# Optimization experiments

Hardware: AMD Instinct MI355X
Metric: run time of the kernel (lower is better)

The kernel has to match this reference:

```python
import jax, jax.numpy as jnp
import numpy as np
import math

B, Q, K, D = 16, 2048, 2048, 128


def setup_inputs() -> dict:
    key = jax.random.key(0)
    k1, k2, k3, k4 = jax.random.split(key, 4)
    return {
        "queries": jax.random.normal(k1, (B, Q, D), dtype=jnp.float32),
        "keys": jax.random.normal(k2, (B, K, D), dtype=jnp.float32),
        "values": jax.random.normal(k3, (B, K, D), dtype=jnp.float32),
        "valid_lens": jax.random.randint(k4, (B,), 1, K + 1, dtype=jnp.int32),
    }


def reference(queries, keys, values, valid_lens):
    d = queries.shape[2]
    # scores: [B, Q, K]
    scores = jnp.einsum("bqd,bkd->bqk", queries, keys) / math.sqrt(d)
    # mask: arange(K) < valid_lens[b], broadcast over query dim -> [B, 1, K]
    mask = jnp.arange(scores.shape[-1])[None, None, :] < valid_lens[:, None, None]
    scores = jnp.where(mask, scores, jnp.float32(-1000000.0))
    weights = jax.nn.softmax(scores, axis=-1)
    return jnp.einsum("bqk,bkd->bqd", weights, values)
```

## Files before the change

kernel.cpp:

```cpp
#include <hip/hip_runtime.h>

typedef unsigned short u16;
typedef __bf16 bf16x8 __attribute__((ext_vector_type(8)));
typedef float f32x4 __attribute__((ext_vector_type(4)));

union B8 { uint4 u; bf16x8 v; };
union U8 { u16 s[8]; uint4 u; };

#define NQ 2048
#define NK 2048
#define ND 128

template<int C>
__device__ __forceinline__ float dppf(float x) {
  int v = __builtin_bit_cast(int, x);
  int r = __builtin_amdgcn_update_dpp(v, v, C, 0xF, 0xF, true);
  return __builtin_bit_cast(float, r);
}
__device__ __forceinline__ float rowmax16(float x) {
  x = fmaxf(x, dppf<0xB1>(x));
  x = fmaxf(x, dppf<0x4E>(x));
  x = fmaxf(x, dppf<0x141>(x));
  x = fmaxf(x, dppf<0x140>(x));
  return x;
}
__device__ __forceinline__ float rowsum16(float x) {
  x += dppf<0xB1>(x);
  x += dppf<0x4E>(x);
  x += dppf<0x141>(x);
  x += dppf<0x140>(x);
  return x;
}

__device__ __forceinline__ bf16x8 cvt8(float4 a, float4 b) {
  bf16x8 r;
  r[0] = (__bf16)a.x; r[1] = (__bf16)a.y; r[2] = (__bf16)a.z; r[3] = (__bf16)a.w;
  r[4] = (__bf16)b.x; r[5] = (__bf16)b.y; r[6] = (__bf16)b.z; r[7] = (__bf16)b.w;
  return r;
}

__device__ __forceinline__ void async16(const u16* g, u16* l) {
  __builtin_amdgcn_global_load_lds(
      (const __attribute__((address_space(1))) unsigned int*)g,
      (__attribute__((address_space(3))) unsigned int*)l, 16, 0, 0);
}

__global__ __launch_bounds__(256)
void prepack(const float* __restrict__ kg, const float* __restrict__ vg,
             u16* __restrict__ wk, u16* __restrict__ wvp)
{
  __shared__ __align__(16) u16 sVp[8192];
  const int bt  = blockIdx.x;
  const int tid = threadIdx.x;
  const int srow = tid >> 2, scq = tid & 3;
  const size_t rowoff = (size_t)((bt >> 5) * NK + (bt & 31) * 64 + srow) * ND + scq * 32;

  u16* kimg = wk + (size_t)bt * 8192;
  {
    const float* src = kg + rowoff;
    #pragma unroll
    for (int c = 0; c < 4; ++c) {
      B8 tt; tt.v = cvt8(*(const float4*)(src + c * 8), *(const float4*)(src + c * 8 + 4));
      *(uint4*)(&kimg[srow * 128 + (((scq * 4 + c) ^ (srow & 15)) << 3)]) = tt.u;
    }
  }
  {
    const float* src = vg + rowoff;
    #pragma unroll
    for (int c = 0; c < 4; ++c) {
      B8 x; x.v = cvt8(*(const float4*)(src + c * 8), *(const float4*)(src + c * 8 + 4));
      U8 tt; tt.u = x.u;
      #pragma unroll
      for (int j = 0; j < 8; ++j) {
        int d = scq * 32 + c * 8 + j;
        sVp[d * 64 + (((srow >> 3) ^ j) << 3) + (srow & 7)] = tt.s[j];
      }
    }
  }
  __syncthreads();
  u16* vimg = wvp + (size_t)bt * 8192;
  const uint4* s4 = (const uint4*)sVp;
  uint4* d4 = (uint4*)vimg;
  #pragma unroll
  for (int k = 0; k < 4; ++k) d4[tid + 256 * k] = s4[tid + 256 * k];
}

__global__ __launch_bounds__(512, 2)
void flash_fwd(const float* __restrict__ qg, const int* __restrict__ vlg,
               float* __restrict__ og,
               const u16* __restrict__ wk, const u16* __restrict__ wvp)
{
  __shared__ __align__(16) u16 smem[81920];
  u16* const sKb = smem;
  u16* const sVb = smem + 32768;
  u16* const sPb = smem + 65536;
  float* const fb = (float*)smem;

  const int tid  = threadIdx.x;
  const int lane = tid & 63;
  const int wv   = tid >> 6;
  const int qw   = wv & 3;
  const int grp  = wv >> 2;
  const int n    = lane & 15;
  const int quad = lane >> 4;

  const int bi = blockIdx.x;
  const int b  = ((bi & 7) << 1) | ((bi >> 3) & 1);
  const int qt = bi >> 4;

  const int vl = vlg[b];
  const int nt = (vl + 63) >> 6;

  const int qrow0 = qt * 128 + qw * 32;

  bf16x8 qf[2][4];
  #pragma unroll
  for (int mb = 0; mb < 2; ++mb)
    #pragma unroll
    for (int c = 0; c < 4; ++c) {
      const float* qp = qg + (size_t)(b * NQ + qrow0 + mb * 16 + n) * ND + c * 32 + quad * 8;
      qf[mb][c] = cvt8(*(const float4*)qp, *(const float4*)(qp + 4));
    }

  f32x4 O[2][8];
  float mst[2][4], lst[2][4];
  #pragma unroll
  for (int mb = 0; mb < 2; ++mb) {
    #pragma unroll
    for (int f = 0; f < 8; ++f) O[mb][f] = (f32x4){0.f, 0.f, 0.f, 0.f};
    #pragma unroll
    for (int r = 0; r < 4; ++r) { mst[mb][r] = -__builtin_inff(); lst[mb][r] = 0.f; }
  }

  #define STAGE(t, buf)                                                        \
    do {                                                                       \
      const size_t io_ = (size_t)(b * 32 + (t)) * 8192 + qw * 2048;            \
      const u16* gk_ = wk  + io_ + lane * 8;                                   \
      const u16* gv_ = wvp + io_ + lane * 8;                                   \
      u16* lk_ = sKb + (grp * 2 + (buf)) * 8192 + qw * 2048;                   \
      u16* lv_ = sVb + (grp * 2 + (buf)) * 8192 + qw * 2048;                   \
      _Pragma("unroll")                                                        \
      for (int j_ = 0; j_ < 4; ++j_) {                                         \
        async16(gk_ + j_ * 512, lk_ + j_ * 512 + lane * 8);                    \
        async16(gv_ + j_ * 512, lv_ + j_ * 512 + lane * 8);                    \
      }                                                                        \
    } while (0)

  u16* const Pw = sPb + wv * 2048;

  constexpr float CEXP = 0.08838834764831845f * 1.44269504088896340f;

  if (grp < nt) STAGE(grp, 0);

  const int NS = (nt + 1) >> 1;
  for (int i = 0; i < NS; ++i) {
    __syncthreads();
    const int t  = 2 * i + grp;
    const int tn = t + 2;
    if (tn < nt) STAGE(tn, (i + 1) & 1);

    if (t < nt) {
      const u16* Kg = sKb + (grp * 2 + (i & 1)) * 8192;
      const u16* Vg = sVb + (grp * 2 + (i & 1)) * 8192;

      f32x4 S[2][4];
      #pragma unroll
      for (int mb = 0; mb < 2; ++mb)
        #pragma unroll
        for (int jn = 0; jn < 4; ++jn) S[mb][jn] = (f32x4){0.f, 0.f, 0.f, 0.f};
      #pragma unroll
      for (int c = 0; c < 4; ++c)
        #pragma unroll
        for (int jn = 0; jn < 4; ++jn) {
          B8 bb;
          bb.u = *(const uint4*)(&Kg[(jn * 16 + n) * 128 + (((c * 4 + quad) ^ n) << 3)]);
          S[0][jn] = __builtin_amdgcn_mfma_f32_16x16x32_bf16(qf[0][c], bb.v, S[0][jn], 0, 0, 0);
          S[1][jn] = __builtin_amdgcn_mfma_f32_16x16x32_bf16(qf[1][c], bb.v, S[1][jn], 0, 0, 0);
        }

      if (t * 64 + 64 > vl) {
        #pragma unroll
        for (int jn = 0; jn < 4; ++jn) {
          const bool msk = (t * 64 + jn * 16 + n) >= vl;
          #pragma unroll
          for (int r = 0; r < 4; ++r) {
            S[0][jn][r] = msk ? -1e30f : S[0][jn][r];
            S[1][jn][r] = msk ? -1e30f : S[1][jn][r];
          }
        }
      }

      float al[2][4];
      #pragma unroll
      for (int mb = 0; mb < 2; ++mb)
        #pragma unroll
        for (int r = 0; r < 4; ++r) {
          float mx = fmaxf(fmaxf(S[mb][0][r], S[mb][1][r]), fmaxf(S[mb][2][r], S[mb][3][r]));
          mx = rowmax16(mx);
          float mnew = fmaxf(mst[mb][r], mx);
          float a = __builtin_exp2f((mst[mb][r] - mnew) * CEXP);
          mst[mb][r] = mnew;
          float ssum = 0.f;
          #pragma unroll
          for (int jn = 0; jn < 4; ++jn) {
            float p = __builtin_exp2f((S[mb][jn][r] - mnew) * CEXP);
            S[mb][jn][r] = p;
            ssum += p;
          }
          ssum = rowsum16(ssum);
          lst[mb][r] = lst[mb][r] * a + ssum;
          al[mb][r] = a;
        }
      #pragma unroll
      for (int mb = 0; mb < 2; ++mb)
        #pragma unroll
        for (int f = 0; f < 8; ++f) {
          O[mb][f][0] *= al[mb][0]; O[mb][f][1] *= al[mb][1];
          O[mb][f][2] *= al[mb][2]; O[mb][f][3] *= al[mb][3];
        }

      #pragma unroll
      for (int mb = 0; mb < 2; ++mb)
        #pragma unroll
        for (int jn = 0; jn < 4; ++jn)
          #pragma unroll
          for (int r = 0; r < 4; ++r) {
            int row = mb * 16 + quad * 4 + r;
            __bf16 h = (__bf16)S[mb][jn][r];
            Pw[row * 64 + (((jn * 2 + (n >> 3)) ^ (row & 7)) << 3) + (n & 7)]
                = __builtin_bit_cast(u16, h);
          }

      #pragma unroll
      for (int kc = 0; kc < 2; ++kc) {
        bf16x8 af[2];
        #pragma unroll
        for (int mb = 0; mb < 2; ++mb) {
          B8 ta;
          ta.u = *(const uint4*)(&Pw[(mb * 16 + n) * 64 + (((kc * 4 + quad) ^ (n & 7)) << 3)]);
          af[mb] = ta.v;
        }
        #pragma unroll
        for (int f = 0; f < 8; ++f) {
          int d = f * 16 + n;
          B8 bb;
          bb.u = *(const uint4*)(&Vg[d * 64 + (((kc * 4 + quad) ^ (n & 7)) << 3)]);
          O[0][f] = __builtin_amdgcn_mfma_f32_16x16x32_bf16(af[0], bb.v, O[0][f], 0, 0, 0);
          O[1][f] = __builtin_amdgcn_mfma_f32_16x16x32_bf16(af[1], bb.v, O[1][f], 0, 0, 0);
        }
      }
    }
  }
  #undef STAGE

  __syncthreads();
  float* const ps = fb + 16384;
  if (grp == 1) {
    #pragma unroll
    for (int mb = 0; mb < 2; ++mb) {
      #pragma unroll
      for (int f = 0; f < 8; ++f)
        #pragma unroll
        for (int r = 0; r < 4; ++r)
          fb[(qw * 32 + mb * 16 + quad * 4 + r) * 128 + f * 16 + n] = O[mb][f][r];
      if (n == 0) {
        #pragma unroll
        for (int r = 0; r < 4; ++r) {
          const int row = qw * 32 + mb * 16 + quad * 4 + r;
          ps[row * 2]     = mst[mb][r];
          ps[row * 2 + 1] = lst[mb][r];
        }
      }
    }
  }
  __syncthreads();
  if (grp == 0) {
    #pragma unroll
    for (int mb = 0; mb < 2; ++mb)
      #pragma unroll
      for (int r = 0; r < 4; ++r) {
        const int row = qw * 32 + mb * 16 + quad * 4 + r;
        const float m1 = ps[row * 2], l1 = ps[row * 2 + 1];
        const float m  = fmaxf(mst[mb][r], m1);
        const float a0 = __builtin_exp2f((mst[mb][r] - m) * CEXP);
        const float a1 = __builtin_exp2f((m1 - m) * CEXP);
        const float rl = 1.0f / (lst[mb][r] * a0 + l1 * a1);
        #pragma unroll
        for (int f = 0; f < 8; ++f) {
          const int idx = row * 128 + f * 16 + n;
          fb[idx] = (O[mb][f][r] * a0 + fb[idx] * a1) * rl;
        }
      }
  }
  __syncthreads();
  {
    const float4* s4 = (const float4*)fb;
    float4* d4 = (float4*)(og + (size_t)(b * NQ + qt * 128) * ND);
    #pragma unroll
    for (int k = 0; k < 8; ++k)
      d4[tid + 512 * k] = s4[tid + 512 * k];
  }
}

__global__ __launch_bounds__(1024)
void flash_fwd_fb(const float* __restrict__ qg, const float* __restrict__ kg,
                  const float* __restrict__ vg, const int* __restrict__ vlg,
                  float* __restrict__ og)
{
  __shared__ __align__(16) u16 sK[2][64 * 128];
  __shared__ __align__(16) u16 sV[2][64 * 128];
  __shared__ __align__(16) u16 sP[16][16 * 64];

  const int tid  = threadIdx.x;
  const int lane = tid & 63;
  const int wv   = tid >> 6;
  const int qw   = wv & 7;
  const int grp  = wv >> 3;
  const int n    = lane & 15;
  const int quad = lane >> 4;

  const int bi = blockIdx.x;
  const int b  = ((bi & 7) << 1) | ((bi >> 3) & 1);
  const int qt = bi >> 4;

  const int vl = vlg[b];
  const int nt = (vl + 63) >> 6;
  const int qrow0 = qt * 128 + qw * 16;

  bf16x8 qf[4];
  #pragma unroll
  for (int c = 0; c < 4; ++c) {
    const float* qp = qg + (size_t)(b * NQ + qrow0 + n) * ND + c * 32 + quad * 8;
    qf[c] = cvt8(*(const float4*)qp, *(const float4*)(qp + 4));
  }

  f32x4 O[8];
  float mst[4], lst[4];
  #pragma unroll
  for (int f = 0; f < 8; ++f) O[f] = (f32x4){0.f, 0.f, 0.f, 0.f};
  #pragma unroll
  for (int r = 0; r < 4; ++r) { mst[r] = -__builtin_inff(); lst[r] = 0.f; }

  const float* kb = kg + (size_t)(b * NK) * ND;
  const float* vb = vg + (size_t)(b * NK) * ND;
  const int stid = tid & 511;
  const int srow = stid >> 3, sc8 = stid & 7;
  bf16x8 kreg[2], vreg[2];

  auto kload = [&](int t) {
    const float* src = kb + (size_t)(t * 64 + srow) * ND + sc8 * 16;
    #pragma unroll
    for (int c = 0; c < 2; ++c)
      kreg[c] = cvt8(*(const float4*)(src + c * 8), *(const float4*)(src + c * 8 + 4));
  };
  auto kstore = [&]() {
    #pragma unroll
    for (int c = 0; c < 2; ++c) {
      B8 tt; tt.v = kreg[c];
      *(uint4*)(&sK[grp][srow * 128 + (((sc8 * 2 + c) ^ (srow & 15)) << 3)]) = tt.u;
    }
  };
  auto vload = [&](int t) {
    const float* src = vb + (size_t)(t * 64 + srow) * ND + sc8 * 16;
    #pragma unroll
    for (int c = 0; c < 2; ++c)
      vreg[c] = cvt8(*(const float4*)(src + c * 8), *(const float4*)(src + c * 8 + 4));
  };
  auto vstore = [&]() {
    #pragma unroll
    for (int c = 0; c < 2; ++c) {
      B8 x; x.v = vreg[c];
      U8 tt; tt.u = x.u;
      #pragma unroll
      for (int j = 0; j < 8; ++j) {
        int d = sc8 * 16 + c * 8 + j;
        sV[grp][d * 64 + (((srow >> 3) ^ j) << 3) + (srow & 7)] = tt.s[j];
      }
    }
  };

  if (grp < nt) { kload(grp); vload(grp); kstore(); vstore(); }

  constexpr float CEXP = 0.08838834764831845f * 1.44269504088896340f;
  u16* Pw = sP[wv];
  const u16* Kg = sK[grp];
  const u16* Vg = sV[grp];

  const int NS = (nt + 1) >> 1;
  for (int i = 0; i < NS; ++i) {
    __syncthreads();
    const int t  = 2 * i + grp;
    const int tn = t + 2;
    if (tn < nt) { kload(tn); vload(tn); }

    if (t < nt) {
      f32x4 S[4];
      #pragma unroll
      for (int jn = 0; jn < 4; ++jn) S[jn] = (f32x4){0.f, 0.f, 0.f, 0.f};
      #pragma unroll
      for (int c = 0; c < 4; ++c)
        #pragma unroll
        for (int jn = 0; jn < 4; ++jn) {
          B8 bb;
          bb.u = *(const uint4*)(&Kg[(jn * 16 + n) * 128 + (((c * 4 + quad) ^ n) << 3)]);
          S[jn] = __builtin_amdgcn_mfma_f32_16x16x32_bf16(qf[c], bb.v, S[jn], 0, 0, 0);
        }
      if (t * 64 + 64 > vl) {
        #pragma unroll
        for (int jn = 0; jn < 4; ++jn) {
          const bool msk = (t * 64 + jn * 16 + n) >= vl;
          #pragma unroll
          for (int r = 0; r < 4; ++r)
            S[jn][r] = msk ? -1e30f : S[jn][r];
        }
      }
      float al[4];
      #pragma unroll
      for (int r = 0; r < 4; ++r) {
        float mx = fmaxf(fmaxf(S[0][r], S[1][r]), fmaxf(S[2][r], S[3][r]));
        mx = rowmax16(mx);
        float mnew = fmaxf(mst[r], mx);
        float a = __builtin_exp2f((mst[r] - mnew) * CEXP);
        mst[r] = mnew;
        float ssum = 0.f;
        #pragma unroll
        for (int jn = 0; jn < 4; ++jn) {
          float p = __builtin_exp2f((S[jn][r] - mnew) * CEXP);
          S[jn][r] = p;
          ssum += p;
        }
        ssum = rowsum16(ssum);
        lst[r] = lst[r] * a + ssum;
        al[r] = a;
      }
      #pragma unroll
      for (int f = 0; f < 8; ++f) {
        O[f][0] *= al[0]; O[f][1] *= al[1]; O[f][2] *= al[2]; O[f][3] *= al[3];
      }
      #pragma unroll
      for (int jn = 0; jn < 4; ++jn)
        #pragma unroll
        for (int r = 0; r < 4; ++r) {
          int row = quad * 4 + r;
          __bf16 h = (__bf16)S[jn][r];
          Pw[row * 64 + (((jn * 2 + (n >> 3)) ^ (row & 7)) << 3) + (n & 7)]
              = __builtin_bit_cast(u16, h);
        }
      #pragma unroll
      for (int kc = 0; kc < 2; ++kc) {
        B8 ta;
        ta.u = *(const uint4*)(&Pw[n * 64 + (((kc * 4 + quad) ^ (n & 7)) << 3)]);
        bf16x8 af = ta.v;
        #pragma unroll
        for (int f = 0; f < 8; ++f) {
          int d = f * 16 + n;
          B8 bb;
          bb.u = *(const uint4*)(&Vg[d * 64 + (((kc * 4 + quad) ^ (n & 7)) << 3)]);
          O[f] = __builtin_amdgcn_mfma_f32_16x16x32_bf16(af, bb.v, O[f], 0, 0, 0);
        }
      }
    }
    __syncthreads();
    if (tn < nt) { kstore(); vstore(); }
  }

  if (grp == 1) {
    float* ob = ((qw < 4) ? (float*)sK : (float*)sV) + (qw & 3) * 2048 + lane * 32;
    #pragma unroll
    for (int f = 0; f < 8; ++f)
      #pragma unroll
      for (int r = 0; r < 4; ++r)
        ob[f * 4 + r] = O[f][r];
    float* sb = (float*)sP + qw * 512 + lane * 8;
    #pragma unroll
    for (int r = 0; r < 4; ++r) { sb[r] = mst[r]; sb[4 + r] = lst[r]; }
  }
  __syncthreads();
  if (grp == 0) {
    const float* ob = ((qw < 4) ? (const float*)sK : (const float*)sV) + (qw & 3) * 2048 + lane * 32;
    const float* sb = (const float*)sP + qw * 512 + lane * 8;
    #pragma unroll
    for (int r = 0; r < 4; ++r) {
      const float m1 = sb[r], l1 = sb[4 + r];
      const float m  = fmaxf(mst[r], m1);
      const float a0 = __builtin_exp2f((mst[r] - m) * CEXP);
      const float a1 = __builtin_exp2f((m1 - m) * CEXP);
      const float rl = 1.0f / (lst[r] * a0 + l1 * a1);
      const int qrow = qrow0 + quad * 4 + r;
      float* op = og + (size_t)(b * NQ + qrow) * ND + n;
      #pragma unroll
      for (int f = 0; f < 8; ++f)
        op[f * 16] = (O[f][r] * a0 + ob[f * 4 + r] * a1) * rl;
    }
  }
}

extern "C" void kernel_launch(void* const* d_in, const int* in_sizes, int n_in,
                              void* d_out, int out_size, void* d_ws, size_t ws_size,
                              hipStream_t stream) {
  const float* q  = (const float*)d_in[0];
  const float* k  = (const float*)d_in[1];
  const float* v  = (const float*)d_in[2];
  const int*  vl  = (const int*)d_in[3];
  float* out = (float*)d_out;

  const size_t need = (size_t)16 * 1024 * 1024;
  if (ws_size >= need) {
    u16* wk  = (u16*)d_ws;
    u16* wvv = wk + 4194304;
    hipLaunchKernelGGL(prepack, dim3(512), dim3(256), 0, stream, k, v, wk, wvv);
    hipLaunchKernelGGL(flash_fwd, dim3(256), dim3(512), 0, stream, q, vl, out, wk, wvv);
  } else {
    hipLaunchKernelGGL(flash_fwd_fb, dim3(256), dim3(1024), 0, stream, q, k, v, vl, out);
  }
}
```

Before: 162.6 us.

## Split attention over key chunks with a separate merge kernel

Adds a split-KV path: flash_chunk processes up to 8 key tiles per block across 1024 blocks, writing partial O plus per-row max and sum to workspace. A merge_chunks kernel then rescales and combines the partials. The aim is to balance work across CUs when valid_lens vary per batch and to raise occupancy, since the old grid of 256 blocks left the whole loop over keys to one block. The cost is an extra kernel launch, fp32 partial traffic through global memory, and a path that only runs when the workspace is large enough.

```diff
diff --git a/kernel.cpp b/kernel.cpp
--- a/kernel.cpp
+++ b/kernel.cpp
@@ -44,6 +44,8 @@
       (const __attribute__((address_space(1))) unsigned int*)g,
       (__attribute__((address_space(3))) unsigned int*)l, 16, 0, 0);
 }
+
+constexpr float CEXP = 0.08838834764831845f * 1.44269504088896340f;
 
 __global__ __launch_bounds__(256)
 void prepack(const float* __restrict__ kg, const float* __restrict__ vg,
@@ -83,6 +85,216 @@
   uint4* d4 = (uint4*)vimg;
   #pragma unroll
   for (int k = 0; k < 4; ++k) d4[tid + 256 * k] = s4[tid + 256 * k];
+}
+
+__global__ __launch_bounds__(512, 4)
+void flash_chunk(const float* __restrict__ qg, const int* __restrict__ vlg,
+                 const u16* __restrict__ wk, const u16* __restrict__ wvp,
+                 float* __restrict__ pO, float* __restrict__ pML)
+{
+  __shared__ __align__(16) u16 sK[2][8192];
+  __shared__ __align__(16) u16 sV[2][8192];
+  __shared__ __align__(16) u16 sP[8][1024];
+
+  const int tid  = threadIdx.x;
+  const int lane = tid & 63;
+  const int wv   = tid >> 6;
+  const int n    = lane & 15;
+  const int quad = lane >> 4;
+
+  const int bi   = blockIdx.x;
+  const int b    = ((bi & 7) << 1) | ((bi >> 3) & 1);
+  const int rest = bi >> 4;
+  const int qt   = rest & 15;
+  const int ck   = rest >> 4;
+
+  const int vl = vlg[b];
+  const int nt = (vl + 63) >> 6;
+  const int t0 = ck * 8;
+  if (t0 >= nt) return;
+  const int t1 = (t0 + 8 < nt) ? (t0 + 8) : nt;
+
+  const int qrow0 = qt * 128 + wv * 16;
+
+  bf16x8 qf[4];
+  #pragma unroll
+  for (int c = 0; c < 4; ++c) {
+    const float* qp = qg + (size_t)(b * NQ + qrow0 + n) * ND + c * 32 + quad * 8;
+    qf[c] = cvt8(*(const float4*)qp, *(const float4*)(qp + 4));
+  }
+
+  f32x4 O[8];
+  float mst[4], lst[4];
+  #pragma unroll
+  for (int f = 0; f < 8; ++f) O[f] = (f32x4){0.f, 0.f, 0.f, 0.f};
+  #pragma unroll
+  for (int r = 0; r < 4; ++r) { mst[r] = -__builtin_inff(); lst[r] = 0.f; }
+
+  #define STAGE(t, buf)                                                        \
+    do {                                                                       \
+      const size_t io_ = (size_t)(b * 32 + (t)) * 8192 + wv * 1024;            \
+      const u16* gk_ = wk  + io_ + lane * 8;                                   \
+      const u16* gv_ = wvp + io_ + lane * 8;                                   \
+      u16* lk_ = sK[(buf)] + wv * 1024 + lane * 8;                             \
+      u16* lv_ = sV[(buf)] + wv * 1024 + lane * 8;                             \
+      async16(gk_,       lk_);                                                 \
+      async16(gk_ + 512, lk_ + 512);                                           \
+      async16(gv_,       lv_);                                                 \
+      async16(gv_ + 512, lv_ + 512);                                           \
+    } while (0)
+
+  u16* const Pw = sP[wv];
+
+  STAGE(t0, 0);
+
+  for (int t = t0; t < t1; ++t) {
+    __syncthreads();
+    if (t + 1 < t1) STAGE(t + 1, (t - t0 + 1) & 1);
+
+    const u16* Kg = sK[(t - t0) & 1];
+    const u16* Vg = sV[(t - t0) & 1];
+
+    f32x4 S[4];
+    #pragma unroll
+    for (int jn = 0; jn < 4; ++jn) S[jn] = (f32x4){0.f, 0.f, 0.f, 0.f};
+    #pragma unroll
+    for (int c = 0; c < 4; ++c)
+      #pragma unroll
+      for (int jn = 0; jn < 4; ++jn) {
+        B8 bb;
+        bb.u = *(const uint4*)(&Kg[(jn * 16 + n) * 128 + (((c * 4 + quad) ^ n) << 3)]);
+        S[jn] = __builtin_amdgcn_mfma_f32_16x16x32_bf16(qf[c], bb.v, S[jn], 0, 0, 0);
+      }
+
+    if (t * 64 + 64 > vl) {
+      #pragma unroll
+      for (int jn = 0; jn < 4; ++jn) {
+        const bool msk = (t * 64 + jn * 16 + n) >= vl;
+        #pragma unroll
+        for (int r = 0; r < 4; ++r)
+          S[jn][r] = msk ? -1e30f : S[jn][r];
+      }
+    }
+
+    float al[4];
+    #pragma unroll
+    for (int r = 0; r < 4; ++r) {
+      float mx = fmaxf(fmaxf(S[0][r], S[1][r]), fmaxf(S[2][r], S[3][r]));
+      mx = rowmax16(mx);
+      float mnew = fmaxf(mst[r], mx);
+      float a = __builtin_exp2f((mst[r] - mnew) * CEXP);
+      mst[r] = mnew;
+      float ssum = 0.f;
+      #pragma unroll
+      for (int jn = 0; jn < 4; ++jn) {
+        float p = __builtin_exp2f((S[jn][r] - mnew) * CEXP);
+        S[jn][r] = p;
+        ssum += p;
+      }
+      ssum = rowsum16(ssum);
+      lst[r] = lst[r] * a + ssum;
+      al[r] = a;
+    }
+    #pragma unroll
+    for (int f = 0; f < 8; ++f) {
+      O[f][0] *= al[0]; O[f][1] *= al[1]; O[f][2] *= al[2]; O[f][3] *= al[3];
+    }
+
+    #pragma unroll
+    for (int jn = 0; jn < 4; ++jn)
+      #pragma unroll
+      for (int r = 0; r < 4; ++r) {
+        int row = quad * 4 + r;
+        __bf16 h = (__bf16)S[jn][r];
+        Pw[row * 64 + (((jn * 2 + (n >> 3)) ^ (row & 7)) << 3) + (n & 7)]
+            = __builtin_bit_cast(u16, h);
+      }
+
+    #pragma unroll
+    for (int kc = 0; kc < 2; ++kc) {
+      B8 ta;
+      ta.u = *(const uint4*)(&Pw[n * 64 + (((kc * 4 + quad) ^ (n & 7)) << 3)]);
+      bf16x8 af = ta.v;
+      #pragma unroll
+      for (int f = 0; f < 8; ++f) {
+        int d = f * 16 + n;
+        B8 bb;
+        bb.u = *(const uint4*)(&Vg[d * 64 + (((kc * 4 + quad) ^ (n & 7)) << 3)]);
+        O[f] = __builtin_amdgcn_mfma_f32_16x16x32_bf16(af, bb.v, O[f], 0, 0, 0);
+      }
+    }
+  }
+  #undef STAGE
+
+  const size_t ti = (size_t)((b * 16 + qt) * 4 + ck);
+  float* po = pO + ti * 16384;
+  #pragma unroll
+  for (int f = 0; f < 8; ++f)
+    #pragma unroll
+    for (int r = 0; r < 4; ++r)
+      po[(wv * 16 + quad * 4 + r) * 128 + f * 16 + n] = O[f][r];
+  if (n == 0) {
+    float* ps = pML + ti * 256;
+    #pragma unroll
+    for (int r = 0; r < 4; ++r) {
+      const int row = wv * 16 + quad * 4 + r;
+      ps[row * 2]     = mst[r];
+      ps[row * 2 + 1] = lst[r];
+    }
+  }
+}
+
+__global__ __launch_bounds__(256)
+void merge_chunks(const int* __restrict__ vlg, const float* __restrict__ pO,
+                  const float* __restrict__ pML, float* __restrict__ og)
+{
+  __shared__ float w[128][4];
+  const int tid = threadIdx.x;
+  const int bi  = blockIdx.x;
+  const int b   = ((bi & 7) << 1) | ((bi >> 3) & 1);
+  const int qt  = bi >> 4;
+
+  const int vl = vlg[b];
+  const int nt = (vl + 63) >> 6;
+  const int nc = (nt + 7) >> 3;
+  const size_t ti0 = (size_t)(b * 16 + qt) * 4;
+
+  if (tid < 128) {
+    const int row = tid;
+    float m[4], l[4];
+    float mx = -__builtin_inff();
+    for (int c = 0; c < nc; ++c) {
+      m[c] = pML[(ti0 + c) * 256 + row * 2];
+      l[c] = pML[(ti0 + c) * 256 + row * 2 + 1];
+      mx = fmaxf(mx, m[c]);
+    }
+    float L = 0.f;
+    float a[4];
+    for (int c = 0; c < nc; ++c) {
+      a[c] = __builtin_exp2f((m[c] - mx) * CEXP);
+      L += l[c] * a[c];
+    }
+    const float inv = 1.0f / L;
+    #pragma unroll
+    for (int c = 0; c < 4; ++c)
+      w[row][c] = (c < nc) ? a[c] * inv : 0.f;
+  }
+  __syncthreads();
+
+  const float4* p4 = (const float4*)(pO + ti0 * 16384);
+  float4* o4 = (float4*)(og + (size_t)(b * NQ + qt * 128) * ND);
+  #pragma unroll
+  for (int it = 0; it < 16; ++it) {
+    const int gi  = it * 256 + tid;
+    const int row = gi >> 5;
+    float4 acc = {0.f, 0.f, 0.f, 0.f};
+    for (int c = 0; c < nc; ++c) {
+      const float4 x = p4[c * 4096 + gi];
+      const float s = w[row][c];
+      acc.x += x.x * s; acc.y += x.y * s; acc.z += x.z * s; acc.w += x.w * s;
+    }
+    o4[gi] = acc;
+  }
 }
 
 __global__ __launch_bounds__(512, 2)
@@ -110,7 +322,6 @@
 
   const int vl = vlg[b];
   const int nt = (vl + 63) >> 6;
-
   const int qrow0 = qt * 128 + qw * 32;
 
   bf16x8 qf[2][4];
@@ -147,8 +358,6 @@
     } while (0)
 
   u16* const Pw = sPb + wv * 2048;
-
-  constexpr float CEXP = 0.08838834764831845f * 1.44269504088896340f;
 
   if (grp < nt) STAGE(grp, 0);
 
@@ -381,7 +590,6 @@
 
   if (grp < nt) { kload(grp); vload(grp); kstore(); vstore(); }
 
-  constexpr float CEXP = 0.08838834764831845f * 1.44269504088896340f;
   u16* Pw = sP[wv];
   const u16* Kg = sK[grp];
   const u16* Vg = sV[grp];
@@ -504,8 +712,20 @@
   const int*  vl  = (const int*)d_in[3];
   float* out = (float*)d_out;
 
-  const size_t need = (size_t)16 * 1024 * 1024;
-  if (ws_size >= need) {
+  const size_t need_img   = (size_t)16 * 1024 * 1024;
+  const size_t need_split = need_img + (size_t)(64 + 1) * 1024 * 1024;
+
+  if (ws_size >= need_split) {
+    u16*   wk  = (u16*)d_ws;
+    u16*   wvv = wk + 4194304;
+    float* pO  = (float*)((char*)d_ws + need_img);
+    float* pML = (float*)((char*)d_ws + need_img + (size_t)64 * 1024 * 1024);
+    hipLaunchKernelGGL(prepack, dim3(512), dim3(256), 0, stream, k, v, wk, wvv);
+    hipLaunchKernelGGL(flash_chunk, dim3(1024), dim3(512), 0, stream,
+                       q, vl, wk, wvv, pO, pML);
+    hipLaunchKernelGGL(merge_chunks, dim3(256), dim3(256), 0, stream,
+                       vl, pO, pML, out);
+  } else if (ws_size >= need_img) {
     u16* wk  = (u16*)d_ws;
     u16* wvv = wk + 4194304;
     hipLaunchKernelGGL(prepack, dim3(512), dim3(256), 0, stream, k, v, wk, wvv);
```

Result: slower. 172.8 us (+6.3%).
